# Optimization experiments

Measured on AMD Instinct MI355X. Metric: run time of the kernel, lower is better.

Reference implementation:

```python
import jax, jax.numpy as jnp
import numpy as np

NUM_USER = 1_000_000
NUM_ITEM = 100_000
HIDDEN = 64
NUM_PAIRS = 2_000_000


def setup_inputs() -> dict:
    key = jax.random.key(0)
    k1, k2, k3, k4 = jax.random.split(key, 4)
    user_emb = jax.random.normal(k1, (NUM_USER, HIDDEN), dtype=jnp.float32)
    item_emb = jax.random.normal(k2, (NUM_ITEM, HIDDEN), dtype=jnp.float32)
    user_ids = jax.random.randint(k3, (NUM_PAIRS,), 0, NUM_USER, dtype=jnp.int32)
    item_ids = jax.random.randint(k4, (NUM_PAIRS,), 0, NUM_ITEM, dtype=jnp.int32)
    return {"user_emb": user_emb, "item_emb": item_emb,
            "user_ids": user_ids, "item_ids": item_ids}


def reference(user_emb, item_emb, user_ids, item_ids):
    # PMF rating prediction: relu(<U[u], V[i]>) for each observed (u, i) pair.
    u = user_emb[user_ids]          # [P, D] gather
    v = item_emb[item_ids]          # [P, D] gather
    ratings = jnp.einsum('pd,pd->p', u, v)  # per-pair dot product
    return jax.nn.relu(ratings)
```

## Files before the change

kernel.cpp:

```cpp
#include <hip/hip_runtime.h>


constexpr int HIDDEN = 64;
constexpr int K = 4;
constexpr int MAX_BUCKETS = 512;
constexpr int BASE_CHUNK = 4096;

using uint = unsigned int;
using u64 = unsigned long long;

__global__ __launch_bounds__(256) void pmf_dot_kernel(
    const float* __restrict__ user_emb,
    const float* __restrict__ item_emb,
    const int*   __restrict__ user_ids,
    const int*   __restrict__ item_ids,
    float*       __restrict__ out,
    int n_pairs)
{
    const int group  = (blockIdx.x * blockDim.x + threadIdx.x) >> 4;
    const int lane16 = threadIdx.x & 15;
    const int p0     = group * K;

    if (p0 + K <= n_pairs) {
        const int4 u4 = *reinterpret_cast<const int4*>(user_ids + p0);
        const int4 i4 = *reinterpret_cast<const int4*>(item_ids + p0);

        const float4* up0 = reinterpret_cast<const float4*>(user_emb + (size_t)u4.x * HIDDEN) + lane16;
        const float4* up1 = reinterpret_cast<const float4*>(user_emb + (size_t)u4.y * HIDDEN) + lane16;
        const float4* up2 = reinterpret_cast<const float4*>(user_emb + (size_t)u4.z * HIDDEN) + lane16;
        const float4* up3 = reinterpret_cast<const float4*>(user_emb + (size_t)u4.w * HIDDEN) + lane16;
        const float4* vp0 = reinterpret_cast<const float4*>(item_emb + (size_t)i4.x * HIDDEN) + lane16;
        const float4* vp1 = reinterpret_cast<const float4*>(item_emb + (size_t)i4.y * HIDDEN) + lane16;
        const float4* vp2 = reinterpret_cast<const float4*>(item_emb + (size_t)i4.z * HIDDEN) + lane16;
        const float4* vp3 = reinterpret_cast<const float4*>(item_emb + (size_t)i4.w * HIDDEN) + lane16;

        const float4 a0 = *up0, a1 = *up1, a2 = *up2, a3 = *up3;
        const float4 b0 = *vp0, b1 = *vp1, b2 = *vp2, b3 = *vp3;

        float d0 = a0.x * b0.x + a0.y * b0.y + a0.z * b0.z + a0.w * b0.w;
        float d1 = a1.x * b1.x + a1.y * b1.y + a1.z * b1.z + a1.w * b1.w;
        float d2 = a2.x * b2.x + a2.y * b2.y + a2.z * b2.z + a2.w * b2.w;
        float d3 = a3.x * b3.x + a3.y * b3.y + a3.z * b3.z + a3.w * b3.w;

        #pragma unroll
        for (int s = 1; s < 16; s <<= 1) {
            d0 += __shfl_xor(d0, s, 16);
            d1 += __shfl_xor(d1, s, 16);
            d2 += __shfl_xor(d2, s, 16);
            d3 += __shfl_xor(d3, s, 16);
        }

        if (lane16 == 0) {
            float4 r;
            r.x = d0 > 0.0f ? d0 : 0.0f;
            r.y = d1 > 0.0f ? d1 : 0.0f;
            r.z = d2 > 0.0f ? d2 : 0.0f;
            r.w = d3 > 0.0f ? d3 : 0.0f;
            *reinterpret_cast<float4*>(out + p0) = r;
        }
    } else if (p0 < n_pairs) {
        for (int p = p0; p < n_pairs; ++p) {
            const int uid = user_ids[p];
            const int iid = item_ids[p];
            const float4 a = *(reinterpret_cast<const float4*>(user_emb + (size_t)uid * HIDDEN) + lane16);
            const float4 b = *(reinterpret_cast<const float4*>(item_emb + (size_t)iid * HIDDEN) + lane16);
            float d = a.x * b.x + a.y * b.y + a.z * b.z + a.w * b.w;
            #pragma unroll
            for (int s = 1; s < 16; s <<= 1) d += __shfl_xor(d, s, 16);
            if (lane16 == 0) out[p] = d > 0.0f ? d : 0.0f;
        }
    }
}

__global__ __launch_bounds__(256) void chunk_hist_kernel(
    const int* __restrict__ uids, uint* __restrict__ chunkhist,
    int n, int chunk, int shift)
{
    __shared__ uint h[MAX_BUCKETS];
    for (int i = threadIdx.x; i < MAX_BUCKETS; i += 256) h[i] = 0u;
    __syncthreads();
    const int start = blockIdx.x * chunk;
    const int end   = min(start + chunk, n);
    const int L     = end - start;
    const int L4    = L & ~3;
    for (int i = start + threadIdx.x * 4; i < start + L4; i += 1024) {
        const int4 u4 = *reinterpret_cast<const int4*>(uids + i);
        atomicAdd(&h[min(((uint)u4.x) >> shift, (uint)(MAX_BUCKETS - 1))], 1u);
        atomicAdd(&h[min(((uint)u4.y) >> shift, (uint)(MAX_BUCKETS - 1))], 1u);
        atomicAdd(&h[min(((uint)u4.z) >> shift, (uint)(MAX_BUCKETS - 1))], 1u);
        atomicAdd(&h[min(((uint)u4.w) >> shift, (uint)(MAX_BUCKETS - 1))], 1u);
    }
    for (int i = start + L4 + threadIdx.x; i < end; i += 256)
        atomicAdd(&h[min(((uint)uids[i]) >> shift, (uint)(MAX_BUCKETS - 1))], 1u);
    __syncthreads();
    for (int i = threadIdx.x; i < MAX_BUCKETS; i += 256)
        chunkhist[(size_t)blockIdx.x * MAX_BUCKETS + i] = h[i];
}

__global__ __launch_bounds__(MAX_BUCKETS) void scanB1_kernel(
    const uint* __restrict__ chunkhist, uint* __restrict__ chunkbase,
    uint* __restrict__ btotal, int nchunks)
{
    __shared__ uint tmp[MAX_BUCKETS];
    const int b = blockIdx.x;
    const int t = threadIdx.x;
    const uint v = (t < nchunks) ? chunkhist[(size_t)t * MAX_BUCKETS + b] : 0u;
    tmp[t] = v;
    __syncthreads();
    #pragma unroll
    for (int d = 1; d < MAX_BUCKETS; d <<= 1) {
        const uint w = (t >= d) ? tmp[t - d] : 0u;
        __syncthreads();
        tmp[t] += w;
        __syncthreads();
    }
    if (t < nchunks)
        chunkbase[(size_t)t * MAX_BUCKETS + b] = tmp[t] - v;
    if (t == MAX_BUCKETS - 1) btotal[b] = tmp[t];
}

__global__ __launch_bounds__(MAX_BUCKETS) void scanB2_kernel(
    const uint* __restrict__ btotal, uint* __restrict__ offsets)
{
    __shared__ uint tmp[MAX_BUCKETS];
    const int t = threadIdx.x;
    tmp[t] = btotal[t];
    __syncthreads();
    #pragma unroll
    for (int d = 1; d < MAX_BUCKETS; d <<= 1) {
        const uint w = (t >= d) ? tmp[t - d] : 0u;
        __syncthreads();
        tmp[t] += w;
        __syncthreads();
    }
    offsets[t] = t ? tmp[t - 1] : 0u;
    if (t == MAX_BUCKETS - 1) offsets[MAX_BUCKETS] = tmp[t];
}

__global__ __launch_bounds__(256) void scatter_kernel(
    const int* __restrict__ uids, const int* __restrict__ iids,
    const uint* __restrict__ chunkbase, const uint* __restrict__ offsets,
    u64* __restrict__ recs, int n, int chunk, int shift, int bits_u, int bits_i)
{
    __shared__ uint base[MAX_BUCKETS];
    __shared__ uint lcnt[MAX_BUCKETS];
    for (int i = threadIdx.x; i < MAX_BUCKETS; i += 256) {
        base[i] = chunkbase[(size_t)blockIdx.x * MAX_BUCKETS + i] + offsets[i];
        lcnt[i] = 0u;
    }
    __syncthreads();
    const int start = blockIdx.x * chunk;
    const int end   = min(start + chunk, n);
    for (int i = start + threadIdx.x; i < end; i += 256) {
        const uint u = (uint)uids[i];
        const uint v = (uint)iids[i];
        const uint b = min(u >> shift, (uint)(MAX_BUCKETS - 1));
        const uint slot = base[b] + atomicAdd(&lcnt[b], 1u);
        if (slot < (uint)n)
            recs[slot] = (u64)u | ((u64)v << bits_u) | ((u64)(uint)i << (bits_u + bits_i));
    }
}

__global__ __launch_bounds__(256) void pmf_binned_kernel(
    const float* __restrict__ user_emb,
    const float* __restrict__ item_emb,
    const uint*  __restrict__ offsets,
    const u64*   __restrict__ recs,
    float*       __restrict__ out,
    int bits_u, int bits_i)
{
    const int bucket = blockIdx.x >> 2;
    const uint s = offsets[bucket];
    const uint e = offsets[bucket + 1];
    const int lane16 = threadIdx.x & 15;
    const int g = ((blockIdx.x & 3) << 4) | (threadIdx.x >> 4);

    const u64 mu = ((u64)1 << bits_u) - 1;
    const u64 mi = ((u64)1 << bits_i) - 1;

    for (uint q = s + (uint)g * 4u; q < e; q += 256u) {
        uint idx = q + (uint)(lane16 & 3);
        if (idx >= e) idx = e - 1;
        const u64 rec = recs[idx];
        const int uu = (int)(rec & mu);
        const int vv = (int)((rec >> bits_u) & mi);

        const int u0 = __shfl(uu, 0, 16), i0 = __shfl(vv, 0, 16);
        const int u1 = __shfl(uu, 1, 16), i1 = __shfl(vv, 1, 16);
        const int u2 = __shfl(uu, 2, 16), i2 = __shfl(vv, 2, 16);
        const int u3 = __shfl(uu, 3, 16), i3 = __shfl(vv, 3, 16);

        const float4* up0 = reinterpret_cast<const float4*>(user_emb + (size_t)u0 * HIDDEN) + lane16;
        const float4* up1 = reinterpret_cast<const float4*>(user_emb + (size_t)u1 * HIDDEN) + lane16;
        const float4* up2 = reinterpret_cast<const float4*>(user_emb + (size_t)u2 * HIDDEN) + lane16;
        const float4* up3 = reinterpret_cast<const float4*>(user_emb + (size_t)u3 * HIDDEN) + lane16;
        const float4* vp0 = reinterpret_cast<const float4*>(item_emb + (size_t)i0 * HIDDEN) + lane16;
        const float4* vp1 = reinterpret_cast<const float4*>(item_emb + (size_t)i1 * HIDDEN) + lane16;
        const float4* vp2 = reinterpret_cast<const float4*>(item_emb + (size_t)i2 * HIDDEN) + lane16;
        const float4* vp3 = reinterpret_cast<const float4*>(item_emb + (size_t)i3 * HIDDEN) + lane16;

        const float4 a0 = *up0, a1 = *up1, a2 = *up2, a3 = *up3;
        const float4 b0 = *vp0, b1 = *vp1, b2 = *vp2, b3 = *vp3;

        float d0 = a0.x * b0.x + a0.y * b0.y + a0.z * b0.z + a0.w * b0.w;
        float d1 = a1.x * b1.x + a1.y * b1.y + a1.z * b1.z + a1.w * b1.w;
        float d2 = a2.x * b2.x + a2.y * b2.y + a2.z * b2.z + a2.w * b2.w;
        float d3 = a3.x * b3.x + a3.y * b3.y + a3.z * b3.z + a3.w * b3.w;

        #pragma unroll
        for (int sft = 1; sft < 16; sft <<= 1) {
            d0 += __shfl_xor(d0, sft, 16);
            d1 += __shfl_xor(d1, sft, 16);
            d2 += __shfl_xor(d2, sft, 16);
            d3 += __shfl_xor(d3, sft, 16);
        }

        if (lane16 < 4 && (q + (uint)lane16) < e) {
            const float d = lane16 == 0 ? d0 : lane16 == 1 ? d1 : lane16 == 2 ? d2 : d3;
            out[(uint)(rec >> (bits_u + bits_i))] = d > 0.0f ? d : 0.0f;
        }
    }
}

extern "C" void kernel_launch(void* const* d_in, const int* in_sizes, int n_in,
                              void* d_out, int out_size, void* d_ws, size_t ws_size,
                              hipStream_t stream) {
    const float* user_emb = (const float*)d_in[0];
    const float* item_emb = (const float*)d_in[1];
    const int*   user_ids = (const int*)d_in[2];
    const int*   item_ids = (const int*)d_in[3];
    float* out = (float*)d_out;

    const int n_pairs = in_sizes[2];

    const long long n_users = (long long)in_sizes[0] / HIDDEN;
    const long long n_items = (long long)in_sizes[1] / HIDDEN;

    int shift = 11;
    while (n_users > 0 && (((n_users - 1) >> shift) >= MAX_BUCKETS)) ++shift;

    auto bits_for = [](long long v) { int b = 1; while ((1ll << b) < v) ++b; return b; };
    const int bits_u = bits_for(n_users > 1 ? n_users : 2);
    const int bits_i = bits_for(n_items > 1 ? n_items : 2);
    const int bits_p = bits_for(n_pairs > 1 ? n_pairs : 2);

    int chunk = BASE_CHUNK;
    while ((n_pairs + chunk - 1) / chunk > MAX_BUCKETS) chunk <<= 1;
    const int nchunks = (n_pairs + chunk - 1) / chunk;

    const size_t META = 8192 + 2ull * MAX_BUCKETS * MAX_BUCKETS * sizeof(uint);
    const size_t ws_need = META + (size_t)n_pairs * sizeof(u64);

    if (d_ws == nullptr || ws_size < ws_need || n_pairs < BASE_CHUNK ||
        bits_u + bits_i + bits_p > 64 || n_users <= 0 || n_items <= 0) {
        const int threads = 256;
        const int pairs_per_block = (threads / 16) * K;
        const int blocks = (n_pairs + pairs_per_block - 1) / pairs_per_block;
        pmf_dot_kernel<<<blocks, threads, 0, stream>>>(
            user_emb, item_emb, user_ids, item_ids, out, n_pairs);
        return;
    }

    uint* offsets   = (uint*)d_ws;
    uint* btotal    = (uint*)((char*)d_ws + 4096);
    uint* chunkhist = (uint*)((char*)d_ws + 8192);
    uint* chunkbase = chunkhist + (size_t)MAX_BUCKETS * MAX_BUCKETS;
    u64*  recs      = (u64*)((char*)d_ws + META);

    chunk_hist_kernel<<<nchunks, 256, 0, stream>>>(
        user_ids, chunkhist, n_pairs, chunk, shift);
    scanB1_kernel<<<MAX_BUCKETS, MAX_BUCKETS, 0, stream>>>(
        chunkhist, chunkbase, btotal, nchunks);
    scanB2_kernel<<<1, MAX_BUCKETS, 0, stream>>>(btotal, offsets);
    scatter_kernel<<<nchunks, 256, 0, stream>>>(
        user_ids, item_ids, chunkbase, offsets, recs, n_pairs, chunk, shift,
        bits_u, bits_i);
    pmf_binned_kernel<<<MAX_BUCKETS * 4, 256, 0, stream>>>(
        user_emb, item_emb, offsets, recs, out, bits_u, bits_i);
}
```

Baseline: 493.0 us.

## Add second-level sub-bucket sort of records by user id within each bucket

Adds a subsort kernel that splits each coarse user bucket into 128 sub-buckets by user id and writes the records into a second workspace buffer, so the binned dot kernel walks user rows in closer to sorted order. The aim is better locality and cache reuse on user embedding gathers. In exchange it adds one kernel launch, an extra read and write pass over the 16 MB record array, and twice the workspace. The new path runs only when the workspace is large enough for the second buffer.

New measurement: 494.9 us. About the same (+0.4%).

```diff
diff --git a/kernel.cpp b/kernel.cpp
--- a/kernel.cpp
+++ b/kernel.cpp
@@ -5,6 +5,7 @@
 constexpr int K = 4;
 constexpr int MAX_BUCKETS = 512;
 constexpr int BASE_CHUNK = 4096;
+constexpr int SUBB = 128;
 
 using uint = unsigned int;
 using u64 = unsigned long long;
@@ -161,6 +162,46 @@
     }
 }
 
+__global__ __launch_bounds__(256) void subsort_kernel(
+    const u64* __restrict__ recs, u64* __restrict__ recs2,
+    const uint* __restrict__ offsets, int subshift, u64 mu)
+{
+    const uint s = offsets[blockIdx.x];
+    const uint e = offsets[blockIdx.x + 1];
+    __shared__ uint h[SUBB];
+    __shared__ uint tmp[SUBB];
+    __shared__ uint base[SUBB];
+    __shared__ uint cnt[SUBB];
+    const int t = threadIdx.x;
+    if (t < SUBB) h[t] = 0u;
+    __syncthreads();
+    for (uint i = s + t; i < e; i += 256) {
+        const uint uid = (uint)(recs[i] & mu);
+        atomicAdd(&h[(uid >> subshift) & (SUBB - 1)], 1u);
+    }
+    __syncthreads();
+    const uint v = (t < SUBB) ? h[t] : 0u;
+    if (t < SUBB) tmp[t] = v;
+    __syncthreads();
+    #pragma unroll
+    for (int d = 1; d < SUBB; d <<= 1) {
+        uint w = 0u;
+        if (t < SUBB && t >= d) w = tmp[t - d];
+        __syncthreads();
+        if (t < SUBB) tmp[t] += w;
+        __syncthreads();
+    }
+    if (t < SUBB) { base[t] = tmp[t] - v; cnt[t] = 0u; }
+    __syncthreads();
+    for (uint i = s + t; i < e; i += 256) {
+        const u64 rec = recs[i];
+        const uint sb = ((uint)(rec & mu) >> subshift) & (SUBB - 1);
+        const uint dst = s + base[sb] + atomicAdd(&cnt[sb], 1u);
+        if (dst < e)
+            recs2[dst] = rec;
+    }
+}
+
 __global__ __launch_bounds__(256) void pmf_binned_kernel(
     const float* __restrict__ user_emb,
     const float* __restrict__ item_emb,
@@ -238,6 +279,7 @@
 
     int shift = 11;
     while (n_users > 0 && (((n_users - 1) >> shift) >= MAX_BUCKETS)) ++shift;
+    const int subshift = shift - 7;
 
     auto bits_for = [](long long v) { int b = 1; while ((1ll << b) < v) ++b; return b; };
     const int bits_u = bits_for(n_users > 1 ? n_users : 2);
@@ -249,10 +291,13 @@
     const int nchunks = (n_pairs + chunk - 1) / chunk;
 
     const size_t META = 8192 + 2ull * MAX_BUCKETS * MAX_BUCKETS * sizeof(uint);
-    const size_t ws_need = META + (size_t)n_pairs * sizeof(u64);
-
-    if (d_ws == nullptr || ws_size < ws_need || n_pairs < BASE_CHUNK ||
-        bits_u + bits_i + bits_p > 64 || n_users <= 0 || n_items <= 0) {
+    const size_t ws_need1 = META + (size_t)n_pairs * sizeof(u64);
+    const size_t ws_need2 = META + 2ull * (size_t)n_pairs * sizeof(u64);
+
+    const bool ok_shape = !(n_pairs < BASE_CHUNK || bits_u + bits_i + bits_p > 64 ||
+                            n_users <= 0 || n_items <= 0);
+
+    if (d_ws == nullptr || ws_size < ws_need1 || !ok_shape) {
         const int threads = 256;
         const int pairs_per_block = (threads / 16) * K;
         const int blocks = (n_pairs + pairs_per_block - 1) / pairs_per_block;
@@ -266,6 +311,9 @@
     uint* chunkhist = (uint*)((char*)d_ws + 8192);
     uint* chunkbase = chunkhist + (size_t)MAX_BUCKETS * MAX_BUCKETS;
     u64*  recs      = (u64*)((char*)d_ws + META);
+    u64*  recs2     = recs + n_pairs;
+
+    const bool do_subsort = (ws_size >= ws_need2) && (subshift >= 0);
 
     chunk_hist_kernel<<<nchunks, 256, 0, stream>>>(
         user_ids, chunkhist, n_pairs, chunk, shift);
@@ -275,6 +323,15 @@
     scatter_kernel<<<nchunks, 256, 0, stream>>>(
         user_ids, item_ids, chunkbase, offsets, recs, n_pairs, chunk, shift,
         bits_u, bits_i);
+
+    const u64* drecs = recs;
+    if (do_subsort) {
+        const u64 mu = ((u64)1 << bits_u) - 1;
+        subsort_kernel<<<MAX_BUCKETS, 256, 0, stream>>>(
+            recs, recs2, offsets, subshift, mu);
+        drecs = recs2;
+    }
+
     pmf_binned_kernel<<<MAX_BUCKETS * 4, 256, 0, stream>>>(
-        user_emb, item_emb, offsets, recs, out, bits_u, bits_i);
-}
+        user_emb, item_emb, offsets, drecs, out, bits_u, bits_i);
+}
```

## Sub-bin records per bucket in LDS before gathering, vectorize scatter loads

Applied to the files above, without the earlier changes.

The compute kernel now runs two blocks per user bucket. Each block takes half of the bucket's records, counting-sorts them in shared memory into 128 finer user sub-bins, and then gathers embeddings in that order, so neighbouring threads touch nearby user rows and get better cache locality. The scatter kernel reads ids as int4 vectors to cut load instructions. The cost is an extra in-block histogram, scan and shuffle with many syncthreads. Blocks drop from 2048 to 1024, and segments longer than 2560 records fall back to global reads.

New measurement: 472.5 us. 4.2% less time.

```diff
diff --git a/kernel.cpp b/kernel.cpp
--- a/kernel.cpp
+++ b/kernel.cpp
@@ -5,6 +5,8 @@
 constexpr int K = 4;
 constexpr int MAX_BUCKETS = 512;
 constexpr int BASE_CHUNK = 4096;
+constexpr int SUBB = 128;
+constexpr int MAXSEG = 2560;
 
 using uint = unsigned int;
 using u64 = unsigned long long;
@@ -151,37 +153,100 @@
     __syncthreads();
     const int start = blockIdx.x * chunk;
     const int end   = min(start + chunk, n);
-    for (int i = start + threadIdx.x; i < end; i += 256) {
+    const int L     = end - start;
+    const int L4    = L & ~3;
+    for (int i = start + threadIdx.x * 4; i < start + L4; i += 1024) {
+        const int4 u4 = *reinterpret_cast<const int4*>(uids + i);
+        const int4 i4 = *reinterpret_cast<const int4*>(iids + i);
+        const int us[4] = {u4.x, u4.y, u4.z, u4.w};
+        const int vs[4] = {i4.x, i4.y, i4.z, i4.w};
+        #pragma unroll
+        for (int k = 0; k < 4; ++k) {
+            const uint u = (uint)us[k];
+            const uint b = min(u >> shift, (uint)(MAX_BUCKETS - 1));
+            const uint slot = base[b] + atomicAdd(&lcnt[b], 1u);
+            if (slot < (uint)n)
+                recs[slot] = (u64)u | ((u64)(uint)vs[k] << bits_u)
+                           | ((u64)(uint)(i + k) << (bits_u + bits_i));
+        }
+    }
+    for (int i = start + L4 + threadIdx.x; i < end; i += 256) {
         const uint u = (uint)uids[i];
-        const uint v = (uint)iids[i];
         const uint b = min(u >> shift, (uint)(MAX_BUCKETS - 1));
         const uint slot = base[b] + atomicAdd(&lcnt[b], 1u);
         if (slot < (uint)n)
-            recs[slot] = (u64)u | ((u64)v << bits_u) | ((u64)(uint)i << (bits_u + bits_i));
-    }
-}
-
-__global__ __launch_bounds__(256) void pmf_binned_kernel(
+            recs[slot] = (u64)u | ((u64)(uint)iids[i] << bits_u)
+                       | ((u64)(uint)i << (bits_u + bits_i));
+    }
+}
+
+__global__ __launch_bounds__(256) void pmf_fused_kernel(
     const float* __restrict__ user_emb,
     const float* __restrict__ item_emb,
     const uint*  __restrict__ offsets,
     const u64*   __restrict__ recs,
     float*       __restrict__ out,
-    int bits_u, int bits_i)
-{
-    const int bucket = blockIdx.x >> 2;
-    const uint s = offsets[bucket];
-    const uint e = offsets[bucket + 1];
-    const int lane16 = threadIdx.x & 15;
-    const int g = ((blockIdx.x & 3) << 4) | (threadIdx.x >> 4);
-
+    int bits_u, int bits_i, int subshift)
+{
+    __shared__ u64  lrec[MAXSEG];
+    __shared__ uint h[SUBB];
+    __shared__ uint tmp[SUBB];
+    __shared__ uint sbase[SUBB];
+    __shared__ uint scnt[SUBB];
+
+    const int  bucket = blockIdx.x >> 1;
+    const int  half   = blockIdx.x & 1;
+    const uint s0 = offsets[bucket];
+    const uint e0 = offsets[bucket + 1];
+    const uint len0 = e0 - s0;
+    const uint mid  = s0 + ((len0 + 1u) >> 1);
+    const uint s   = half ? mid : s0;
+    const uint e   = half ? e0  : mid;
+    const uint len = (e > s) ? (e - s) : 0u;
+
+    const int t = threadIdx.x;
     const u64 mu = ((u64)1 << bits_u) - 1;
     const u64 mi = ((u64)1 << bits_i) - 1;
 
-    for (uint q = s + (uint)g * 4u; q < e; q += 256u) {
+    const bool use_lds = (len > 0u) && (len <= (uint)MAXSEG);
+    if (use_lds) {
+        if (t < SUBB) h[t] = 0u;
+        __syncthreads();
+        for (uint i = (uint)t; i < len; i += 256u) {
+            const uint uid = (uint)(recs[s + i] & mu);
+            atomicAdd(&h[(uid >> subshift) & (SUBB - 1)], 1u);
+        }
+        __syncthreads();
+        const uint v = (t < SUBB) ? h[t] : 0u;
+        if (t < SUBB) tmp[t] = v;
+        __syncthreads();
+        #pragma unroll
+        for (int d = 1; d < SUBB; d <<= 1) {
+            uint w = 0u;
+            if (t < SUBB && t >= d) w = tmp[t - d];
+            __syncthreads();
+            if (t < SUBB) tmp[t] += w;
+            __syncthreads();
+        }
+        if (t < SUBB) { sbase[t] = tmp[t] - v; scnt[t] = 0u; }
+        __syncthreads();
+        for (uint i = (uint)t; i < len; i += 256u) {
+            const u64 r = recs[s + i];
+            const uint sb = ((uint)(r & mu) >> subshift) & (SUBB - 1);
+            const uint dst = sbase[sb] + atomicAdd(&scnt[sb], 1u);
+            if (dst < (uint)MAXSEG)
+                lrec[dst] = r;
+        }
+        __syncthreads();
+    }
+
+    const int lane16 = t & 15;
+    const int g = t >> 4;
+
+    for (uint q = (uint)g * 4u; q < len; q += 64u) {
         uint idx = q + (uint)(lane16 & 3);
-        if (idx >= e) idx = e - 1;
-        const u64 rec = recs[idx];
+        if (idx >= len) idx = len - 1u;
+        const u64 rec = use_lds ? lrec[idx] : recs[s + idx];
         const int uu = (int)(rec & mu);
         const int vv = (int)((rec >> bits_u) & mi);
 
@@ -215,7 +280,7 @@
             d3 += __shfl_xor(d3, sft, 16);
         }
 
-        if (lane16 < 4 && (q + (uint)lane16) < e) {
+        if (lane16 < 4 && (q + (uint)lane16) < len) {
             const float d = lane16 == 0 ? d0 : lane16 == 1 ? d1 : lane16 == 2 ? d2 : d3;
             out[(uint)(rec >> (bits_u + bits_i))] = d > 0.0f ? d : 0.0f;
         }
@@ -238,6 +303,7 @@
 
     int shift = 11;
     while (n_users > 0 && (((n_users - 1) >> shift) >= MAX_BUCKETS)) ++shift;
+    const int subshift = shift - 7;
 
     auto bits_for = [](long long v) { int b = 1; while ((1ll << b) < v) ++b; return b; };
     const int bits_u = bits_for(n_users > 1 ? n_users : 2);
@@ -251,8 +317,10 @@
     const size_t META = 8192 + 2ull * MAX_BUCKETS * MAX_BUCKETS * sizeof(uint);
     const size_t ws_need = META + (size_t)n_pairs * sizeof(u64);
 
-    if (d_ws == nullptr || ws_size < ws_need || n_pairs < BASE_CHUNK ||
-        bits_u + bits_i + bits_p > 64 || n_users <= 0 || n_items <= 0) {
+    const bool ok_shape = !(n_pairs < BASE_CHUNK || bits_u + bits_i + bits_p > 64 ||
+                            n_users <= 0 || n_items <= 0 || subshift < 0);
+
+    if (d_ws == nullptr || ws_size < ws_need || !ok_shape) {
         const int threads = 256;
         const int pairs_per_block = (threads / 16) * K;
         const int blocks = (n_pairs + pairs_per_block - 1) / pairs_per_block;
@@ -275,6 +343,6 @@
     scatter_kernel<<<nchunks, 256, 0, stream>>>(
         user_ids, item_ids, chunkbase, offsets, recs, n_pairs, chunk, shift,
         bits_u, bits_i);
-    pmf_binned_kernel<<<MAX_BUCKETS * 4, 256, 0, stream>>>(
-        user_emb, item_emb, offsets, recs, out, bits_u, bits_i);
-}
+    pmf_fused_kernel<<<MAX_BUCKETS * 2, 256, 0, stream>>>(
+        user_emb, item_emb, offsets, recs, out, bits_u, bits_i, subshift);
+}
```
